# Kernel optimization log

Measured on AMD Instinct MI355X. Metric: run time of the kernel, lower is better.

Reference implementation:

```python
import jax, jax.numpy as jnp
import numpy as np

N, E, F, H, C, K = 50000, 1600000, 128, 64, 40, 4


def setup_inputs() -> dict:
    key = jax.random.key(0)
    ks = jax.random.split(key, 4)
    x = jax.random.normal(ks[0], (N, F), dtype=jnp.float32)
    edge_index = jax.random.randint(ks[1], (2, E), 0, N, dtype=jnp.int32)
    edge_weight = jnp.ones((E,), dtype=jnp.float32)
    # lin of ChebConv: Linear(K*in, out); kaiming for layer1, xavier-ish for layer2
    W1 = jax.random.normal(ks[2], (K * F, H), dtype=jnp.float32) * (2.0 / (K * F)) ** 0.5
    b1 = jnp.zeros((H,), jnp.float32)
    W2 = jax.random.normal(ks[3], (K * H, C), dtype=jnp.float32) * (2.0 / (K * H + C)) ** 0.5
    b2 = jnp.zeros((C,), jnp.float32)
    return {"x": x, "edge_index": edge_index, "edge_weight": edge_weight,
            "W1": W1, "b1": b1, "W2": W2, "b2": b2}


def _cheb_norm(edge_index, edge_weight, num_nodes):
    """Edge weights of L_hat = 2*L/lambda_max - I with sym norm, lambda_max=2.
    L = I - D^{-1/2} A D^{-1/2}; so L_hat off-diag = -d_i^{-1/2} w d_j^{-1/2},
    diag = (1 if deg>0 else 0) - 1."""
    src, dst = edge_index[0], edge_index[1]
    deg = jax.ops.segment_sum(edge_weight, src, num_segments=num_nodes)
    dis = jnp.where(deg > 0, jax.lax.rsqrt(jnp.maximum(deg, 1e-12)), 0.0)
    w_norm = -dis[src] * edge_weight * dis[dst]   # [E] off-diagonal of L_hat
    diag = jnp.where(deg > 0, 0.0, -1.0)          # [N] diagonal of L_hat
    return src, dst, w_norm, diag


def _cheb_conv(x, src, dst, w_norm, diag, W, b, num_nodes):
    def prop(h):  # L_hat @ h via gather-multiply-scatter
        msg = w_norm[:, None] * h[src]                                  # [E, F]
        return diag[:, None] * h + jax.ops.segment_sum(msg, dst, num_segments=num_nodes)

    Tx_prev2 = x
    Tx_prev1 = prop(x)
    Txs = [Tx_prev2, Tx_prev1]
    for _ in range(2, K):
        Tx = 2.0 * prop(Tx_prev1) - Tx_prev2
        Txs.append(Tx)
        Tx_prev2, Tx_prev1 = Tx_prev1, Tx
    Z = jnp.concatenate(Txs, axis=1)              # [N, K*F]
    return Z @ W + b


def reference(x, edge_index, edge_weight, W1, b1, W2, b2):
    num_nodes = x.shape[0]
    src, dst, w_norm, diag = _cheb_norm(edge_index, edge_weight, num_nodes)
    # dropout layers are identity at inference
    h = _cheb_conv(x, src, dst, w_norm, diag, W1, b1, num_nodes)
    h = jax.nn.relu(h)
    out = _cheb_conv(h, src, dst, w_norm, diag, W2, b2, num_nodes)
    return out
```

## Files before the change

kernel.cpp:

```cpp
#include <hip/hip_runtime.h>

#define NN 50000
#define EE 1600000
#define FF 128
#define HH 64
#define CC 40

#define NCH 64
#define CHE (EE / NCH)
#define NSL 4
#define SLN (NN / NSL)

#define PA 250
#define EPP (EE / PA)
#define SB 250
#define SLNB 200
#define BCAP 64

static __device__ __forceinline__ float bf2f(unsigned short u) {
    union { unsigned int i; float f; } c; c.i = ((unsigned int)u) << 16; return c.f;
}
static __device__ __forceinline__ unsigned short f2bf(float x) {
    union { float f; unsigned int i; } c; c.f = x;
    unsigned int r = c.i + 0x7FFFu + ((c.i >> 16) & 1u);
    return (unsigned short)(r >> 16);
}

typedef __attribute__((ext_vector_type(8))) short bf16x8;
typedef __attribute__((ext_vector_type(4))) float f32x4;
union BF8 { bf16x8 v; unsigned short u[8]; };

__global__ __launch_bounds__(1024) void deg_hist_kernel(
    const int* __restrict__ src, const float* __restrict__ w,
    float* __restrict__ pdeg) {
    __shared__ float ldeg[SLN];
    int s = blockIdx.x % NSL;
    int c = blockIdx.x / NSL;
    int base = s * SLN;
    for (int i = threadIdx.x; i < SLN; i += 1024) ldeg[i] = 0.f;
    __syncthreads();
    int e0 = c * CHE;
    for (int e = e0 + threadIdx.x; e < e0 + CHE; e += 1024) {
        int se = src[e];
        unsigned us = (unsigned)(se - base);
        if (us < SLN) atomicAdd(&ldeg[us], w[e]);
    }
    __syncthreads();
    for (int i = threadIdx.x; i < SLN; i += 1024)
        pdeg[(size_t)c * NN + base + i] = ldeg[i];
}

__global__ void reduce_kernel(const float* __restrict__ pdeg,
                              float* __restrict__ dis, float* __restrict__ diag) {
    int n = blockIdx.x * blockDim.x + threadIdx.x;
    if (n >= NN) return;
    float dsum = 0.f;
    for (int c = 0; c < NCH; ++c) dsum += pdeg[(size_t)c * NN + n];
    dis[n]  = (dsum > 0.f) ? rsqrtf(fmaxf(dsum, 1e-12f)) : 0.f;
    diag[n] = (dsum > 0.f) ? 0.f : -1.f;
}

__global__ __launch_bounds__(256) void bucketA_kernel(
    const int* __restrict__ src, const int* __restrict__ dst,
    const float* __restrict__ w, const float* __restrict__ dis,
    uint2* __restrict__ buckets, int* __restrict__ counts) {
    __shared__ int lcnt[SB];
    int p = blockIdx.x;
    for (int i = threadIdx.x; i < SB; i += 256) lcnt[i] = 0;
    __syncthreads();
    int e0 = p * EPP;
    for (int e = e0 + threadIdx.x; e < e0 + EPP; e += 256) {
        int de = dst[e], se = src[e];
        int sl = de / SLNB;
        int dl = de - sl * SLNB;
        float wn = -dis[se] * w[e] * dis[de];
        unsigned lo = (unsigned)se | ((unsigned)f2bf(wn) << 16);
        int idx = atomicAdd(&lcnt[sl], 1);
        buckets[((size_t)p * SB + sl) * BCAP + idx] = make_uint2(lo, (unsigned)dl);
    }
    __syncthreads();
    for (int i = threadIdx.x; i < SB; i += 256) counts[p * SB + i] = lcnt[i];
}

__global__ void scanS_kernel(const int* __restrict__ counts, int* __restrict__ sbase) {
    __shared__ int sh[256];
    int t = threadIdx.x;
    int total = 0;
    if (t < SB)
        for (int p = 0; p < PA; ++p) total += counts[p * SB + t];
    sh[t] = total;
    __syncthreads();
    for (int off = 1; off < 256; off <<= 1) {
        int x = (t >= off) ? sh[t - off] : 0;
        __syncthreads();
        sh[t] += x;
        __syncthreads();
    }
    if (t < SB) sbase[t] = sh[t] - total;
    if (t == SB - 1) sbase[SB] = sh[t];
}

__global__ __launch_bounds__(256) void bucketB_kernel(
    const uint2* __restrict__ buckets, const int* __restrict__ counts,
    const int* __restrict__ sbase,
    int* __restrict__ row_start, unsigned int* __restrict__ csr) {
    __shared__ int lcounts[PA];
    __shared__ int lhist[SLNB];
    __shared__ int sh[256];
    int s = blockIdx.x;
    int t = threadIdx.x;
    if (t < PA) lcounts[t] = counts[t * SB + s];
    for (int i = t; i < SLNB; i += 256) lhist[i] = 0;
    __syncthreads();
    int g = t >> 4, l16 = t & 15;
    for (int p = g; p < PA; p += 16) {
        int c = lcounts[p];
        const uint2* b = buckets + ((size_t)p * SB + s) * BCAP;
        for (int i = l16; i < c; i += 16)
            atomicAdd(&lhist[b[i].y], 1);
    }
    __syncthreads();
    int v = (t < SLNB) ? lhist[t] : 0;
    sh[t] = v;
    __syncthreads();
    for (int off = 1; off < 256; off <<= 1) {
        int x = (t >= off) ? sh[t - off] : 0;
        __syncthreads();
        sh[t] += x;
        __syncthreads();
    }
    int base = sbase[s];
    if (t < SLNB) {
        int excl = sh[t] - v;
        row_start[s * SLNB + t] = base + excl;
        lhist[t] = base + excl;
    }
    if (s == SB - 1 && t == 0) row_start[NN] = sbase[SB];
    __syncthreads();
    for (int p = g; p < PA; p += 16) {
        int c = lcounts[p];
        const uint2* b = buckets + ((size_t)p * SB + s) * BCAP;
        for (int i = l16; i < c; i += 16) {
            uint2 en = b[i];
            int pos = atomicAdd(&lhist[en.y], 1);
            csr[pos] = en.x;
        }
    }
}

template <int FACT, typename OUT_T>
__global__ __launch_bounds__(256) void prop2_kernel(
    const unsigned short* __restrict__ a, float alphaL,
    const unsigned short* __restrict__ p1, float beta1,
    const unsigned short* __restrict__ p2, float beta2,
    const float* __restrict__ bias, int doRelu, int FOUT, int outStride,
    const float* __restrict__ diag, const int* __restrict__ rs,
    const unsigned int* __restrict__ csr, OUT_T* __restrict__ out) {
    int lane = threadIdx.x & 63;
    int wave = threadIdx.x >> 6;
    int n = blockIdx.x * 4 + wave;
    int f = lane;
    float acc = 0.f;
    if (f < FACT) {
        acc = diag[n] * bf2f(a[(size_t)n * 64 + f]);
        int j0 = rs[n], j1 = rs[n + 1];
        int j = j0;
        for (; j + 8 <= j1; j += 8) {
            unsigned cw[8];
            #pragma unroll
            for (int u = 0; u < 8; ++u) cw[u] = csr[j + u];
            float v[8];
            #pragma unroll
            for (int u = 0; u < 8; ++u)
                v[u] = bf2f(a[(size_t)(cw[u] & 0xFFFFu) * 64 + f]);
            #pragma unroll
            for (int u = 0; u < 8; ++u)
                acc = fmaf(bf2f((unsigned short)(cw[u] >> 16)), v[u], acc);
        }
        for (; j < j1; ++j) {
            unsigned cw = csr[j];
            acc = fmaf(bf2f((unsigned short)(cw >> 16)),
                       bf2f(a[(size_t)(cw & 0xFFFFu) * 64 + f]), acc);
        }
    }
    if (f < FOUT) {
        float r = alphaL * acc + beta1 * bf2f(p1[(size_t)n * 64 + f]);
        if (beta2 != 0.f) r = fmaf(beta2, bf2f(p2[(size_t)n * 64 + f]), r);
        if (bias) r += bias[f];
        if (doRelu) r = fmaxf(r, 0.f);
        OUT_T o;
        if constexpr (sizeof(OUT_T) == 2) o = f2bf(r); else o = r;
        out[(size_t)n * outStride + f] = o;
    }
}

__global__ __launch_bounds__(256) void convw_kernel(
    const float* __restrict__ W1, const float* __restrict__ W2,
    unsigned short* __restrict__ W1t_hi, unsigned short* __restrict__ W1t_lo,
    unsigned short* __restrict__ W2t_hi, unsigned short* __restrict__ W2t_lo) {
    int tid = blockIdx.x * 256 + threadIdx.x;
    if (tid < 512 * 64) {
        int row = tid >> 7, kk = tid & 127;
        int ct = row >> 6, j = row & 63;
        float v = W1[((size_t)(ct * 128 + kk)) * 64 + j];
        unsigned short h = f2bf(v);
        W1t_hi[tid] = h;
        W1t_lo[tid] = f2bf(v - bf2f(h));
    } else {
        int t2 = tid - 512 * 64;
        if (t2 >= 4 * 64 * 64) return;
        int row = t2 >> 6, kk = t2 & 63;
        int kt = row >> 6, j = row & 63;
        float v = (j < CC) ? W2[((size_t)(kt * 64 + kk)) * CC + j] : 0.f;
        unsigned short h = f2bf(v);
        W2t_hi[t2] = h;
        W2t_lo[t2] = f2bf(v - bf2f(h));
    }
}

template <int KF>
__global__ __launch_bounds__(256) void gemm_mfma_kernel(
    const float* __restrict__ A, const unsigned short* __restrict__ Wt_hi,
    const unsigned short* __restrict__ Wt_lo, unsigned short* __restrict__ Yb) {
    constexpr int KK = KF * 32;
    int lane = threadIdx.x & 63;
    int ct   = threadIdx.x >> 6;
    int l15  = lane & 15;
    int lg   = lane >> 4;
    int m0   = blockIdx.x * 32;

    f32x4 acc[2][4];
    #pragma unroll
    for (int i = 0; i < 2; ++i)
        #pragma unroll
        for (int j = 0; j < 4; ++j)
            acc[i][j] = (f32x4){0.f, 0.f, 0.f, 0.f};

    #pragma unroll
    for (int kf = 0; kf < KF; ++kf) {
        int k0 = kf * 32 + lg * 8;
        BF8 bh[4], bl[4];
        #pragma unroll
        for (int nf = 0; nf < 4; ++nf) {
            size_t addr = (size_t)(ct * 64 + nf * 16 + l15) * KK + k0;
            bh[nf].v = *reinterpret_cast<const bf16x8*>(Wt_hi + addr);
            bl[nf].v = *reinterpret_cast<const bf16x8*>(Wt_lo + addr);
        }
        BF8 ah[2], al[2];
        #pragma unroll
        for (int ms = 0; ms < 2; ++ms) {
            int n = m0 + ms * 16 + l15;
            if (n >= NN) n = NN - 1;
            const float* ap = A + (size_t)n * KK + k0;
            float4 f0 = *(const float4*)(ap);
            float4 f1 = *(const float4*)(ap + 4);
            float fv[8] = {f0.x, f0.y, f0.z, f0.w, f1.x, f1.y, f1.z, f1.w};
            #pragma unroll
            for (int u = 0; u < 8; ++u) {
                unsigned short h = f2bf(fv[u]);
                ah[ms].u[u] = h;
                al[ms].u[u] = f2bf(fv[u] - bf2f(h));
            }
        }
        #pragma unroll
        for (int ms = 0; ms < 2; ++ms)
            #pragma unroll
            for (int nf = 0; nf < 4; ++nf) {
                acc[ms][nf] = __builtin_amdgcn_mfma_f32_16x16x32_bf16(
                    ah[ms].v, bh[nf].v, acc[ms][nf], 0, 0, 0);
                acc[ms][nf] = __builtin_amdgcn_mfma_f32_16x16x32_bf16(
                    ah[ms].v, bl[nf].v, acc[ms][nf], 0, 0, 0);
                acc[ms][nf] = __builtin_amdgcn_mfma_f32_16x16x32_bf16(
                    al[ms].v, bh[nf].v, acc[ms][nf], 0, 0, 0);
            }
    }

    unsigned short* slab = Yb + (size_t)ct * NN * 64;
    #pragma unroll
    for (int ms = 0; ms < 2; ++ms)
        #pragma unroll
        for (int r = 0; r < 4; ++r) {
            int n = m0 + ms * 16 + lg * 4 + r;
            if (n < NN) {
                #pragma unroll
                for (int nf = 0; nf < 4; ++nf)
                    slab[(size_t)n * 64 + nf * 16 + l15] = f2bf(acc[ms][nf][r]);
            }
        }
}

extern "C" void kernel_launch(void* const* d_in, const int* in_sizes, int n_in,
                              void* d_out, int out_size, void* d_ws, size_t ws_size,
                              hipStream_t stream) {
    const float* x    = (const float*)d_in[0];
    const int*   eidx = (const int*)d_in[1];
    const float* ew   = (const float*)d_in[2];
    const float* W1   = (const float*)d_in[3];
    const float* b1   = (const float*)d_in[4];
    const float* W2   = (const float*)d_in[5];
    const float* b2   = (const float*)d_in[6];
    float* out = (float*)d_out;

    const int* src = eidx;
    const int* dst = eidx + EE;

    float* p = (float*)d_ws;
    unsigned int* csr = (unsigned int*)p;  p += (size_t)EE;
    float* dis  = p;                  p += ((NN + 63) / 64) * 64;
    float* diag = p;                  p += ((NN + 63) / 64) * 64;
    unsigned short* Yb = (unsigned short*)p;  p += (size_t)NN * 128;
    unsigned short* u  = (unsigned short*)p;  p += (size_t)NN * 32;
    unsigned short* v  = (unsigned short*)p;  p += (size_t)NN * 32;
    float* h    = p;                  p += (size_t)NN * 64;
    float* scratch = p;               p += (size_t)PA * SB * BCAP * 2;
    int* row_start = (int*)p;
    int* counts    = row_start + NN + 1;
    int* sbase     = counts + PA * SB;

    float* pdeg    = scratch;
    uint2* buckets = (uint2*)scratch;
    unsigned short* W1t_hi = (unsigned short*)scratch;
    unsigned short* W1t_lo = W1t_hi + 512 * 64;
    unsigned short* W2t_hi = W1t_lo + 512 * 64;
    unsigned short* W2t_lo = W2t_hi + 4 * 64 * 64;
    unsigned short* y0b = Yb;
    unsigned short* y1b = Yb + (size_t)1 * NN * 64;
    unsigned short* y2b = Yb + (size_t)2 * NN * 64;
    unsigned short* y3b = Yb + (size_t)3 * NN * 64;
    unsigned short* Zb = Yb;
    unsigned short* z0 = Zb;
    unsigned short* z1 = Zb + (size_t)1 * NN * 64;
    unsigned short* z2 = Zb + (size_t)2 * NN * 64;
    unsigned short* z3 = Zb + (size_t)3 * NN * 64;
    unsigned short* u2 = u;
    unsigned short* v2 = v;

    const int B = 256;
    deg_hist_kernel<<<NCH * NSL, 1024, 0, stream>>>(src, ew, pdeg);
    reduce_kernel<<<(NN + B - 1) / B, B, 0, stream>>>(pdeg, dis, diag);
    bucketA_kernel<<<PA, 256, 0, stream>>>(src, dst, ew, dis, buckets, counts);
    scanS_kernel<<<1, 256, 0, stream>>>(counts, sbase);
    bucketB_kernel<<<SB, 256, 0, stream>>>(buckets, counts, sbase, row_start, csr);
    convw_kernel<<<192, 256, 0, stream>>>(W1, W2, W1t_hi, W1t_lo, W2t_hi, W2t_lo);

    int pgrid = NN / 4;
    int ggrid = (NN + 31) / 32;

    gemm_mfma_kernel<4><<<ggrid, 256, 0, stream>>>(x, W1t_hi, W1t_lo, Yb);
    prop2_kernel<64, unsigned short><<<pgrid, 256, 0, stream>>>(
        y3b, 4.f, y2b, 2.f, nullptr, 0.f,
        nullptr, 0, 64, 64, diag, row_start, csr, u);
    prop2_kernel<64, unsigned short><<<pgrid, 256, 0, stream>>>(
        u, 1.f, y1b, 1.f, y3b, -3.f,
        nullptr, 0, 64, 64, diag, row_start, csr, v);
    prop2_kernel<64, float><<<pgrid, 256, 0, stream>>>(
        v, 1.f, y0b, 1.f, y2b, -1.f,
        b1, 1, 64, 64, diag, row_start, csr, h);

    gemm_mfma_kernel<2><<<ggrid, 256, 0, stream>>>(h, W2t_hi, W2t_lo, Zb);
    prop2_kernel<48, unsigned short><<<pgrid, 256, 0, stream>>>(
        z3, 4.f, z2, 2.f, nullptr, 0.f,
        nullptr, 0, 48, 64, diag, row_start, csr, u2);
    prop2_kernel<48, unsigned short><<<pgrid, 256, 0, stream>>>(
        u2, 1.f, z1, 1.f, z3, -3.f,
        nullptr, 0, 48, 64, diag, row_start, csr, v2);
    prop2_kernel<48, float><<<pgrid, 256, 0, stream>>>(
        v2, 1.f, z0, 1.f, z2, -1.f,
        b2, 0, 40, 40, diag, row_start, csr, out);
}
```

Measured before the change: 520.2 us.

## Split feature slabs into 32-wide halves for propagation locality

Stores each GEMM output slab as two half-planes of 32 features per node, and rewrites the propagation kernel so each block handles one half-plane for several nodes (8 nodes per block at 32 lanes each, or 16 at 16 lanes for the 16-wide tail of layer 2). Block ids are interleaved so the two halves are processed concurrently, each over a smaller gather working set. The goal is better L2 hit rates on the random neighbour gathers and no idle lanes in the 48-wide layer-2 passes. The second GEMM reads the half-plane layout of h directly. The cost is more complex indexing, and each node's CSR row is read twice, once per half.

```diff
diff --git a/kernel.cpp b/kernel.cpp
--- a/kernel.cpp
+++ b/kernel.cpp
@@ -16,6 +16,8 @@
 #define SB 250
 #define SLNB 200
 #define BCAP 64
+
+#define HALFE ((size_t)NN * 32)
 
 static __device__ __forceinline__ float bf2f(unsigned short u) {
     union { unsigned int i; float f; } c; c.i = ((unsigned int)u) << 16; return c.f;
@@ -148,49 +150,60 @@
     }
 }
 
-template <int FACT, typename OUT_T>
-__global__ __launch_bounds__(256) void prop2_kernel(
+template <int FACT, typename OUT_T, int FINAL>
+__global__ __launch_bounds__(256) void prop3_kernel(
     const unsigned short* __restrict__ a, float alphaL,
     const unsigned short* __restrict__ p1, float beta1,
     const unsigned short* __restrict__ p2, float beta2,
-    const float* __restrict__ bias, int doRelu, int FOUT, int outStride,
+    const float* __restrict__ bias, int doRelu,
     const float* __restrict__ diag, const int* __restrict__ rs,
     const unsigned int* __restrict__ csr, OUT_T* __restrict__ out) {
-    int lane = threadIdx.x & 63;
-    int wave = threadIdx.x >> 6;
-    int n = blockIdx.x * 4 + wave;
-    int f = lane;
-    float acc = 0.f;
-    if (f < FACT) {
-        acc = diag[n] * bf2f(a[(size_t)n * 64 + f]);
-        int j0 = rs[n], j1 = rs[n + 1];
-        int j = j0;
-        for (; j + 8 <= j1; j += 8) {
-            unsigned cw[8];
-            #pragma unroll
-            for (int u = 0; u < 8; ++u) cw[u] = csr[j + u];
-            float v[8];
-            #pragma unroll
-            for (int u = 0; u < 8; ++u)
-                v[u] = bf2f(a[(size_t)(cw[u] & 0xFFFFu) * 64 + f]);
-            #pragma unroll
-            for (int u = 0; u < 8; ++u)
-                acc = fmaf(bf2f((unsigned short)(cw[u] >> 16)), v[u], acc);
-        }
-        for (; j < j1; ++j) {
-            unsigned cw = csr[j];
-            acc = fmaf(bf2f((unsigned short)(cw >> 16)),
-                       bf2f(a[(size_t)(cw & 0xFFFFu) * 64 + f]), acc);
-        }
-    }
-    if (f < FOUT) {
-        float r = alphaL * acc + beta1 * bf2f(p1[(size_t)n * 64 + f]);
-        if (beta2 != 0.f) r = fmaf(beta2, bf2f(p2[(size_t)n * 64 + f]), r);
-        if (bias) r += bias[f];
-        if (doRelu) r = fmaxf(r, 0.f);
+
+    int bid = blockIdx.x;
+    int x = bid & 7, g = bid >> 3;
+    int pss, nb, F, logF;
+    if constexpr (FACT == 64) {
+        pss = x >> 2; nb = g * 4 + (x & 3); F = 32; logF = 5;
+        if (nb >= NN / 8) return;
+    } else {
+        if (x < 5) { pss = 0; nb = g * 5 + x;       F = 32; logF = 5; if (nb >= NN / 8)  return; }
+        else       { pss = 1; nb = g * 3 + (x - 5); F = 16; logF = 4; if (nb >= NN / 16) return; }
+    }
+    int t = threadIdx.x;
+    int f = t & (F - 1);
+    int node = nb * (256 >> logF) + (t >> logF);
+    const unsigned short* ah = a + (size_t)pss * HALFE;
+
+    float acc = diag[node] * bf2f(ah[(size_t)node * 32 + f]);
+    int j = rs[node], j1 = rs[node + 1];
+    for (; j + 8 <= j1; j += 8) {
+        unsigned cw[8];
+        #pragma unroll
+        for (int u = 0; u < 8; ++u) cw[u] = csr[j + u];
+        float v[8];
+        #pragma unroll
+        for (int u = 0; u < 8; ++u)
+            v[u] = bf2f(ah[(size_t)(cw[u] & 0xFFFFu) * 32 + f]);
+        #pragma unroll
+        for (int u = 0; u < 8; ++u)
+            acc = fmaf(bf2f((unsigned short)(cw[u] >> 16)), v[u], acc);
+    }
+    for (; j < j1; ++j) {
+        unsigned cw = csr[j];
+        acc = fmaf(bf2f((unsigned short)(cw >> 16)),
+                   bf2f(ah[(size_t)(cw & 0xFFFFu) * 32 + f]), acc);
+    }
+    int fg = pss * 32 + f;
+    float r = alphaL * acc + beta1 * bf2f(p1[(size_t)pss * HALFE + (size_t)node * 32 + f]);
+    if (beta2 != 0.f) r = fmaf(beta2, bf2f(p2[(size_t)pss * HALFE + (size_t)node * 32 + f]), r);
+    if (bias) r += bias[fg];
+    if (doRelu) r = fmaxf(r, 0.f);
+    if constexpr (FINAL) {
+        if (fg < CC) ((float*)out)[(size_t)node * CC + fg] = r;
+    } else {
         OUT_T o;
         if constexpr (sizeof(OUT_T) == 2) o = f2bf(r); else o = r;
-        out[(size_t)n * outStride + f] = o;
+        out[(size_t)pss * HALFE + (size_t)node * 32 + f] = o;
     }
 }
 
@@ -218,7 +231,7 @@
     }
 }
 
-template <int KF>
+template <int KF, int AHALF>
 __global__ __launch_bounds__(256) void gemm_mfma_kernel(
     const float* __restrict__ A, const unsigned short* __restrict__ Wt_hi,
     const unsigned short* __restrict__ Wt_lo, unsigned short* __restrict__ Yb) {
@@ -251,7 +264,11 @@
         for (int ms = 0; ms < 2; ++ms) {
             int n = m0 + ms * 16 + l15;
             if (n >= NN) n = NN - 1;
-            const float* ap = A + (size_t)n * KK + k0;
+            const float* ap;
+            if constexpr (AHALF)
+                ap = A + (size_t)kf * HALFE + (size_t)n * 32 + lg * 8;
+            else
+                ap = A + (size_t)n * KK + k0;
             float4 f0 = *(const float4*)(ap);
             float4 f1 = *(const float4*)(ap + 4);
             float fv[8] = {f0.x, f0.y, f0.z, f0.w, f1.x, f1.y, f1.z, f1.w};
@@ -284,7 +301,8 @@
             if (n < NN) {
                 #pragma unroll
                 for (int nf = 0; nf < 4; ++nf)
-                    slab[(size_t)n * 64 + nf * 16 + l15] = f2bf(acc[ms][nf][r]);
+                    slab[(size_t)(nf >> 1) * HALFE + (size_t)n * 32 + (nf & 1) * 16 + l15]
+                        = f2bf(acc[ms][nf][r]);
             }
         }
 }
@@ -343,28 +361,29 @@
     bucketB_kernel<<<SB, 256, 0, stream>>>(buckets, counts, sbase, row_start, csr);
     convw_kernel<<<192, 256, 0, stream>>>(W1, W2, W1t_hi, W1t_lo, W2t_hi, W2t_lo);
 
-    int pgrid = NN / 4;
     int ggrid = (NN + 31) / 32;
-
-    gemm_mfma_kernel<4><<<ggrid, 256, 0, stream>>>(x, W1t_hi, W1t_lo, Yb);
-    prop2_kernel<64, unsigned short><<<pgrid, 256, 0, stream>>>(
+    const int PG64 = 1563 * 8;
+    const int PG48 = 1250 * 8;
+
+    gemm_mfma_kernel<4, 0><<<ggrid, 256, 0, stream>>>(x, W1t_hi, W1t_lo, Yb);
+    prop3_kernel<64, unsigned short, 0><<<PG64, 256, 0, stream>>>(
         y3b, 4.f, y2b, 2.f, nullptr, 0.f,
-        nullptr, 0, 64, 64, diag, row_start, csr, u);
-    prop2_kernel<64, unsigned short><<<pgrid, 256, 0, stream>>>(
+        nullptr, 0, diag, row_start, csr, u);
+    prop3_kernel<64, unsigned short, 0><<<PG64, 256, 0, stream>>>(
         u, 1.f, y1b, 1.f, y3b, -3.f,
-        nullptr, 0, 64, 64, diag, row_start, csr, v);
-    prop2_kernel<64, float><<<pgrid, 256, 0, stream>>>(
+        nullptr, 0, diag, row_start, csr, v);
+    prop3_kernel<64, float, 0><<<PG64, 256, 0, stream>>>(
         v, 1.f, y0b, 1.f, y2b, -1.f,
-        b1, 1, 64, 64, diag, row_start, csr, h);
-
-    gemm_mfma_kernel<2><<<ggrid, 256, 0, stream>>>(h, W2t_hi, W2t_lo, Zb);
-    prop2_kernel<48, unsigned short><<<pgrid, 256, 0, stream>>>(
+        b1, 1, diag, row_start, csr, h);
+
+    gemm_mfma_kernel<2, 1><<<ggrid, 256, 0, stream>>>(h, W2t_hi, W2t_lo, Zb);
+    prop3_kernel<48, unsigned short, 0><<<PG48, 256, 0, stream>>>(
         z3, 4.f, z2, 2.f, nullptr, 0.f,
-        nullptr, 0, 48, 64, diag, row_start, csr, u2);
-    prop2_kernel<48, unsigned short><<<pgrid, 256, 0, stream>>>(
+        nullptr, 0, diag, row_start, csr, u2);
+    prop3_kernel<48, unsigned short, 0><<<PG48, 256, 0, stream>>>(
         u2, 1.f, z1, 1.f, z3, -3.f,
-        nullptr, 0, 48, 64, diag, row_start, csr, v2);
-    prop2_kernel<48, float><<<pgrid, 256, 0, stream>>>(
+        nullptr, 0, diag, row_start, csr, v2);
+    prop3_kernel<48, float, 1><<<PG48, 256, 0, stream>>>(
         v2, 1.f, z0, 1.f, z2, -1.f,
-        b2, 0, 40, 40, diag, row_start, csr, out);
-}
+        b2, 0, diag, row_start, csr, (float*)out);
+}
```

After: 513.3 us. Within noise of the previous version (-1.3%).
